# Optimization experiments

Hardware: AMD Instinct MI355X
Metric: run time of the kernel (lower is better)

The kernel has to match this reference:

```python
import jax, jax.numpy as jnp
import numpy as np

B, S, H, NH = 4, 2048, 512, 8
HD = H // NH  # head dim = 64


def setup_inputs() -> dict:
    key = jax.random.key(0)
    ks = jax.random.split(key, 12)
    f = lambda k, sh: jax.random.normal(k, sh, dtype=jnp.float32)
    w = lambda k: f(k, (H, H)) * 0.02  # Linear weight (out, in), torch-style
    return {
        "q": f(ks[0], (B, S, H)),
        "k": f(ks[1], (B, S, H)),
        "v": f(ks[2], (B, S, H)),
        "mask": jax.random.randint(ks[3], (B, S, S), 0, 2, dtype=jnp.int32),
        "Wq": w(ks[4]), "bq": jnp.zeros((H,), jnp.float32),
        "Wk": w(ks[5]), "bk": jnp.zeros((H,), jnp.float32),
        "Wv": w(ks[6]), "bv": jnp.zeros((H,), jnp.float32),
        "Wo": w(ks[7]), "bo": jnp.zeros((H,), jnp.float32),
    }


def reference(q, k, v, mask, Wq, bq, Wk, bk, Wv, bv, Wo, bo):
    b, s, h = q.shape
    scale = jnp.asarray(np.sqrt(HD), q.dtype)
    # QKV projections (torch Linear: x @ W.T + b), split into heads: b n s h
    def heads(x, W, bias):
        y = x @ W.T + bias
        return y.reshape(b, s, NH, HD).transpose(0, 2, 1, 3)
    Q = heads(q, Wq, bq)
    K = heads(k, Wk, bk)
    V = heads(v, Wv, bv)
    scores = jnp.einsum('bnsh,bnth->bnst', Q, K) / scale
    scores = jnp.where(mask[:, None, :, :] == 0, jnp.asarray(-1e9, scores.dtype), scores)
    attn = jax.nn.softmax(scores, axis=-1)
    # dropout is identity in eval mode
    out = jnp.einsum('bnst,bnth->bnsh', attn, V)
    out = out.transpose(0, 2, 1, 3).reshape(b, s, h)
    return out @ Wo.T + bo
```

## Files before the change

kernel.cpp:

```cpp
#include <hip/hip_runtime.h>
#include <cstdint>


typedef __bf16 bf16x8 __attribute__((ext_vector_type(8)));
typedef float  f32x4  __attribute__((ext_vector_type(4)));
typedef float  f32x16 __attribute__((ext_vector_type(16)));
typedef unsigned int uint32x2 __attribute__((ext_vector_type(2)));

#define MFMA16(a, b, c) __builtin_amdgcn_mfma_f32_16x16x32_bf16(a, b, c, 0, 0, 0)
#define MFMA32(a, b, c) __builtin_amdgcn_mfma_f32_32x32x16_bf16(a, b, c, 0, 0, 0)

__device__ __forceinline__ ushort f2bf(float f) {
  union { float f; uint32_t u; } v; v.f = f;
  return (ushort)((v.u + 0x8000u) >> 16);
}
__device__ __forceinline__ uint packbf(float a, float b) {
  union { float f; uint32_t u; } x, y; x.f = a; y.f = b;
#if __has_builtin(__builtin_amdgcn_perm)
  return __builtin_amdgcn_perm(y.u + 0x8000u, x.u + 0x8000u, 0x07060302u);
#else
  return ((x.u + 0x8000u) >> 16) | ((y.u + 0x8000u) & 0xffff0000u);
#endif
}
__device__ __forceinline__ uint cvtpk(float a, float b) {
  uint r;
  asm("v_cvt_pk_bf16_f32 %0, %1, %2" : "=v"(r) : "v"(a), "v"(b));
  return r;
}
__device__ __forceinline__ float exp2r(float x) {
#if __has_builtin(__builtin_amdgcn_exp2f)
  return __builtin_amdgcn_exp2f(x);
#else
  return exp2f(x);
#endif
}

typedef const __attribute__((address_space(1))) unsigned int* gas_u32;
typedef __attribute__((address_space(3))) unsigned int* las_u32;
__device__ __forceinline__ void gll16(const void* g, void* l) {
  __builtin_amdgcn_global_load_lds((gas_u32)g, (las_u32)l, 16, 0, 0);
}

__global__ __launch_bounds__(256) void cvt_w(
    const float* __restrict__ w0, const float* __restrict__ w1,
    const float* __restrict__ w2, const float* __restrict__ w3,
    ushort* __restrict__ dst) {
  const float* src = (blockIdx.y == 0) ? w0 : (blockIdx.y == 1) ? w1
                   : (blockIdx.y == 2) ? w2 : w3;
  ushort* d = dst + (size_t)blockIdx.y * 262144;
  int i = blockIdx.x * 256 + threadIdx.x;
  for (int j = i; j < 65536; j += 16384) {
    float4 v = ((const float4*)src)[j];
    uint2 o = { packbf(v.x, v.y), packbf(v.z, v.w) };
    ((uint2*)d)[j] = o;
  }
}

__global__ __launch_bounds__(256) void cvt_x(
    const float* __restrict__ q, const float* __restrict__ k,
    const float* __restrict__ v, ushort* __restrict__ dst) {
  const float* src = (blockIdx.y == 0) ? q : (blockIdx.y == 1) ? k : v;
  ushort* d = dst + (size_t)blockIdx.y * 4194304;
  int i = blockIdx.x * 256 + threadIdx.x;
  for (int j = i; j < 1048576; j += 65536) {
    float4 vv = ((const float4*)src)[j];
    uint2 o = { cvtpk(vv.x, vv.y), cvtpk(vv.z, vv.w) };
    ((uint2*)d)[j] = o;
  }
}

__global__ __launch_bounds__(256) void mask_bits_kernel(
    const int* __restrict__ mask, unsigned long long* __restrict__ MB) {
  const int lane = threadIdx.x & 63;
  const int wv = (int)((blockIdx.x * 256 + threadIdx.x) >> 6);
  const size_t base = (size_t)wv * 64;
  for (int j = 0; j < 64; j += 4) {
    int v0 = mask[(base + j + 0) * 64 + lane];
    int v1 = mask[(base + j + 1) * 64 + lane];
    int v2 = mask[(base + j + 2) * 64 + lane];
    int v3 = mask[(base + j + 3) * 64 + lane];
    unsigned long long b0 = __ballot(v0 != 0), b1 = __ballot(v1 != 0);
    unsigned long long b2 = __ballot(v2 != 0), b3 = __ballot(v3 != 0);
    if (lane == 0) {
      MB[base + j] = b0; MB[base + j + 1] = b1;
      MB[base + j + 2] = b2; MB[base + j + 3] = b3;
    }
  }
}

__global__ __launch_bounds__(256, 4) void qkv_gemm(
    const ushort* __restrict__ Xb, const ushort* __restrict__ Wb,
    const float* __restrict__ bq, const float* __restrict__ bk,
    const float* __restrict__ bv, ushort* __restrict__ Qh,
    ushort* __restrict__ Kh, ushort* __restrict__ Vt) {
  __shared__ ushort SM[16384];
  ushort* As = SM;
  ushort* Wt = SM + 8192;
  const int z = blockIdx.z;
  const ushort* X = Xb + (size_t)z * 4194304;
  const ushort* W = Wb + (size_t)z * 262144;
  const float* bias = (z == 0) ? bq : (z == 1) ? bk : bv;
  const float scale = (z == 0) ? 0.18033688011112042f : 1.0f;
  ushort* Y = (z == 0) ? Qh : (z == 1) ? Kh : Vt;

  const int tid = threadIdx.x, wv = tid >> 6, l = tid & 63;
  const int quad = l >> 4, ln = l & 15;
  const int m0 = blockIdx.x * 128, n0 = blockIdx.y * 128;
  const int wm = (wv & 1) * 64, wn = (wv >> 1) * 64;
  const int sr = l >> 3, sc = l & 7;
  f32x4 acc[4][4] = {};

  for (int kk = 0; kk < 512; kk += 64) {
#pragma unroll
    for (int i = 0; i < 4; ++i) {
      int row = wv * 32 + i * 8 + sr;
      gll16(X + (size_t)(m0 + row) * 512 + kk + ((sc ^ (row & 7)) * 8),
            As + (wv * 32 + i * 8) * 64);
      gll16(W + (size_t)(n0 + row) * 512 + kk + ((sc ^ (row & 7)) * 8),
            Wt + (wv * 32 + i * 8) * 64);
    }
    __syncthreads();
#pragma unroll
    for (int ks = 0; ks < 2; ++ks) {
      bf16x8 a[4], bw[4];
#pragma unroll
      for (int mt = 0; mt < 4; ++mt) {
        int row = wm + mt * 16 + ln;
        a[mt] = *(const bf16x8*)&As[row * 64 + (((ks * 4 + quad) ^ (row & 7)) * 8)];
      }
#pragma unroll
      for (int nt = 0; nt < 4; ++nt) {
        int row = wn + nt * 16 + ln;
        bw[nt] = *(const bf16x8*)&Wt[row * 64 + (((ks * 4 + quad) ^ (row & 7)) * 8)];
      }
#pragma unroll
      for (int mt = 0; mt < 4; ++mt)
#pragma unroll
        for (int nt = 0; nt < 4; ++nt)
          acc[mt][nt] = MFMA16(a[mt], bw[nt], acc[mt][nt]);
    }
    __syncthreads();
  }
  float bval[4];
#pragma unroll
  for (int nt = 0; nt < 4; ++nt) bval[nt] = bias[n0 + wn + nt * 16 + ln];

  if (z == 2) {
    ushort* uT = SM;
#pragma unroll
    for (int nt = 0; nt < 4; ++nt) {
      int row = wn + nt * 16 + ln;
#pragma unroll
      for (int mt = 0; mt < 4; ++mt) {
        int mbase = wm + mt * 16 + quad * 4;
        uint2 pk = { cvtpk(acc[mt][nt][0] + bval[nt], acc[mt][nt][1] + bval[nt]),
                     cvtpk(acc[mt][nt][2] + bval[nt], acc[mt][nt][3] + bval[nt]) };
        int c = (mbase >> 3) ^ (row & 7);
        *(uint2*)&uT[row * 128 + c * 8 + (quad & 1) * 4] = pk;
      }
    }
    __syncthreads();
#pragma unroll
    for (int j = 0; j < 8; ++j) {
      int i = tid + j * 256;
      int row = i >> 4, cs = i & 15;
      int g = cs ^ (row & 7);
      uint4 d = *(const uint4*)&uT[row * 128 + cs * 8];
      int n = n0 + row, m = m0 + g * 8;
      int bb = m >> 11, s = m & 2047, h = n >> 6, hd = n & 63;
      *(uint4*)(Y + ((size_t)((bb * 8 + h) * 64 + hd)) * 2048 + s) = d;
    }
  } else {
    ushort* uM = SM;
#pragma unroll
    for (int half = 0; half < 2; ++half) {
      __syncthreads();
      if ((wv >> 1) == half) {
#pragma unroll
        for (int mt = 0; mt < 4; ++mt)
#pragma unroll
          for (int nt = 0; nt < 4; ++nt) {
            int n = nt * 16 + ln;
#pragma unroll
            for (int r = 0; r < 4; ++r) {
              int m = wm + mt * 16 + quad * 4 + r;
              uM[m * 68 + n] = f2bf((acc[mt][nt][r] + bval[nt]) * scale);
            }
          }
      }
      __syncthreads();
#pragma unroll
      for (int j = 0; j < 4; ++j) {
        int i = tid + j * 256;
        int row = i >> 3, cs = i & 7;
        uint4 d = *(const uint4*)&uM[row * 68 + cs * 8];
        int m = m0 + row, n = n0 + half * 64 + cs * 8;
        int bb = m >> 11, s = m & 2047, h = n >> 6, hd = n & 63;
        *(uint4*)(Y + (((size_t)(bb * 8 + h) * 2048) + s) * 64 + hd) = d;
      }
    }
  }
}

__global__ __launch_bounds__(256, 4) void attn(
    const ushort* __restrict__ Qh, const ushort* __restrict__ Kh,
    const ushort* __restrict__ Vt, const unsigned long long* __restrict__ MB,
    ushort* __restrict__ O) {
  __shared__ ushort SMEM[16384];
  ushort* Ks = SMEM;
  ushort* Vs = SMEM + 8192;
  const int tid = threadIdx.x, wv = tid >> 6, lane = tid & 63;
  const int hs = lane >> 5, lq = lane & 31;
  const int qh = wv >> 1, kvh = wv & 1;
  const int bh = blockIdx.x, qb = blockIdx.y;
  const size_t hoff = (size_t)bh * 2048 * 64;
  const int q0 = qb * 64;
  const int qg = q0 + qh * 32 + lq;
  const int srK = lane >> 3, scK = lane & 7;
  const int srV = lane >> 4, scV = lane & 15;

  bf16x8 qf[4];
#pragma unroll
  for (int ki = 0; ki < 4; ++ki)
    qf[ki] = *(const bf16x8*)(Qh + hoff + (size_t)qg * 64 + ki * 16 + hs * 8);

  bf16x8 ones;
#pragma unroll
  for (int j = 0; j < 8; ++j) ones[j] = (__bf16)1.0f;

  f32x16 po0 = {}, po1 = {};
  f32x16 lacc = {};
  const unsigned long long* mrow = MB + ((size_t)(bh >> 3) * 2048 + qg) * 32;

  for (int it = 0; it < 16; ++it) {
    const int kv0 = it * 128;
#pragma unroll
    for (int i = 0; i < 4; ++i) {
      int row = wv * 32 + i * 8 + srK;
      gll16(Kh + hoff + (size_t)(kv0 + row) * 64 + ((scK ^ (row & 7)) * 8),
            Ks + (wv * 32 + i * 8) * 64);
      int rv = wv * 16 + i * 4 + srV;
      gll16(Vt + hoff + (size_t)rv * 2048 + kv0 + ((scV ^ (rv & 7)) * 8),
            Vs + (wv * 16 + i * 4) * 128);
    }
    unsigned long long mbw = mrow[it * 2 + kvh];
    __syncthreads();

#pragma unroll
    for (int ch = 0; ch < 2; ++ch) {
      const int kvb = kvh * 64 + ch * 32;
      f32x16 sc_ = {};
#pragma unroll
      for (int ki = 0; ki < 4; ++ki) {
        int row = kvb + lq;
        bf16x8 ak = *(const bf16x8*)&Ks[row * 64 + (((2 * ki + hs) ^ (row & 7)) * 8)];
        sc_ = MFMA32(ak, qf[ki], sc_);
      }
      uint pk[8];
#pragma unroll
      for (int c = 0; c < 4; ++c) {
        unsigned nib = (unsigned)(mbw >> (ch * 32 + c * 8 + hs * 4)) & 0xFu;
        float p0 = (nib & 1u) ? exp2r(sc_[4 * c + 0]) : 0.f;
        float p1 = (nib & 2u) ? exp2r(sc_[4 * c + 1]) : 0.f;
        float p2 = (nib & 4u) ? exp2r(sc_[4 * c + 2]) : 0.f;
        float p3 = (nib & 8u) ? exp2r(sc_[4 * c + 3]) : 0.f;
        pk[2 * c + 0] = cvtpk(p0, p1);
        pk[2 * c + 1] = cvtpk(p2, p3);
      }
#pragma unroll
      for (int t2 = 0; t2 < 2; ++t2) {
        union { uint u[4]; bf16x8 v; } bp;
#if __has_builtin(__builtin_amdgcn_permlane32_swap)
        uint32x2 r02 = __builtin_amdgcn_permlane32_swap(pk[4 * t2 + 0], pk[4 * t2 + 2], false, false);
        uint32x2 r13 = __builtin_amdgcn_permlane32_swap(pk[4 * t2 + 1], pk[4 * t2 + 3], false, false);
        bp.u[0] = r02[0];
        bp.u[1] = r13[0];
        bp.u[2] = r02[1];
        bp.u[3] = r13[1];
#else
        uint bx0 = (uint)__shfl_xor((int)(hs ? pk[4 * t2 + 0] : pk[4 * t2 + 2]), 32);
        uint bx1 = (uint)__shfl_xor((int)(hs ? pk[4 * t2 + 1] : pk[4 * t2 + 3]), 32);
        bp.u[0] = hs ? bx0 : pk[4 * t2 + 0];
        bp.u[1] = hs ? bx1 : pk[4 * t2 + 1];
        bp.u[2] = hs ? pk[4 * t2 + 2] : bx0;
        bp.u[3] = hs ? pk[4 * t2 + 3] : bx1;
#endif
        lacc = MFMA32(ones, bp.v, lacc);
#pragma unroll
        for (int m2 = 0; m2 < 2; ++m2) {
          int hd = m2 * 32 + lq;
          int gch = (kvb >> 3) + 2 * t2 + hs;
          bf16x8 av = *(const bf16x8*)&Vs[hd * 128 + ((gch ^ (hd & 7)) * 8)];
          if (m2 == 0) po0 = MFMA32(av, bp.v, po0);
          else         po1 = MFMA32(av, bp.v, po1);
        }
      }
    }
    __syncthreads();
  }

  float l_own = lacc[0];
  float* psh = (float*)Ks;
  float* lsh = (float*)Vs;
  ushort* Osh = Vs + 256;
  if (kvh == 1) {
#pragma unroll
    for (int i = 0; i < 16; ++i) psh[(qh * 32 + i) * 64 + lane] = po0[i];
#pragma unroll
    for (int i = 0; i < 16; ++i) psh[(qh * 32 + 16 + i) * 64 + lane] = po1[i];
    lsh[qh * 64 + lane] = l_own;
  }
  __syncthreads();
  if (kvh == 0) {
    float linv = 1.0f / (l_own + lsh[qh * 64 + lane]);
    int row = qh * 32 + lq;
#pragma unroll
    for (int m2 = 0; m2 < 2; ++m2) {
#pragma unroll
      for (int c = 0; c < 4; ++c)
#pragma unroll
        for (int b2 = 0; b2 < 2; ++b2) {
          int r = 4 * c + 2 * b2;
          float v0, v1;
          if (m2 == 0) {
            v0 = (po0[r] + psh[(qh * 32 + r) * 64 + lane]) * linv;
            v1 = (po0[r + 1] + psh[(qh * 32 + r + 1) * 64 + lane]) * linv;
          } else {
            v0 = (po1[r] + psh[(qh * 32 + 16 + r) * 64 + lane]) * linv;
            v1 = (po1[r + 1] + psh[(qh * 32 + 16 + r + 1) * 64 + lane]) * linv;
          }
          int hd = m2 * 32 + 8 * c + 4 * hs + 2 * b2;
          *(uint*)&Osh[row * 72 + hd] = cvtpk(v0, v1);
        }
    }
  }
  __syncthreads();
  for (int i = tid; i < 512; i += 256) {
    int row = i >> 3, cc = i & 7;
    uint4 d = *(const uint4*)&Osh[row * 72 + cc * 8];
    *(uint4*)(O + ((size_t)((bh >> 3) * 2048 + q0 + row)) * 512 +
              (bh & 7) * 64 + cc * 8) = d;
  }
}

__global__ __launch_bounds__(256) void out_gemm(
    const ushort* __restrict__ X, const ushort* __restrict__ W,
    const float* __restrict__ bias, float* __restrict__ Y) {
  __shared__ ushort As[64 * 64];
  __shared__ ushort Ws[128 * 64];
  const int tid = threadIdx.x, wv = tid >> 6, l = tid & 63;
  const int quad = l >> 4, ln = l & 15;
  const int m0 = blockIdx.x * 64, n0 = blockIdx.y * 128;
  const int wm = (wv & 1) * 32, wn = (wv >> 1) * 64;
  const int sr = l >> 3, sc = l & 7;
  f32x4 acc[2][4] = {};
  for (int kk = 0; kk < 512; kk += 64) {
#pragma unroll
    for (int i = 0; i < 2; ++i) {
      int row = wv * 16 + i * 8 + sr;
      gll16(X + (size_t)(m0 + row) * 512 + kk + ((sc ^ (row & 7)) * 8),
            As + (wv * 16 + i * 8) * 64);
    }
#pragma unroll
    for (int i = 0; i < 4; ++i) {
      int row = wv * 32 + i * 8 + sr;
      gll16(W + (size_t)(n0 + row) * 512 + kk + ((sc ^ (row & 7)) * 8),
            Ws + (wv * 32 + i * 8) * 64);
    }
    __syncthreads();
#pragma unroll
    for (int ks = 0; ks < 2; ++ks) {
      bf16x8 a[2], bw[4];
#pragma unroll
      for (int mt = 0; mt < 2; ++mt) {
        int row = wm + mt * 16 + ln;
        a[mt] = *(const bf16x8*)&As[row * 64 + (((ks * 4 + quad) ^ (row & 7)) * 8)];
      }
#pragma unroll
      for (int nt = 0; nt < 4; ++nt) {
        int row = wn + nt * 16 + ln;
        bw[nt] = *(const bf16x8*)&Ws[row * 64 + (((ks * 4 + quad) ^ (row & 7)) * 8)];
      }
#pragma unroll
      for (int mt = 0; mt < 2; ++mt)
#pragma unroll
        for (int nt = 0; nt < 4; ++nt)
          acc[mt][nt] = MFMA16(a[mt], bw[nt], acc[mt][nt]);
    }
    __syncthreads();
  }
#pragma unroll
  for (int mt = 0; mt < 2; ++mt)
#pragma unroll
    for (int nt = 0; nt < 4; ++nt) {
      int n = n0 + wn + nt * 16 + ln;
      float bval = bias[n];
#pragma unroll
      for (int r = 0; r < 4; ++r) {
        int m = m0 + wm + mt * 16 + quad * 4 + r;
        Y[(size_t)m * 512 + n] = acc[mt][nt][r] + bval;
      }
    }
}

extern "C" void kernel_launch(void* const* d_in, const int* in_sizes, int n_in,
                              void* d_out, int out_size, void* d_ws, size_t ws_size,
                              hipStream_t stream) {
  const float* q    = (const float*)d_in[0];
  const float* k    = (const float*)d_in[1];
  const float* v    = (const float*)d_in[2];
  const int*   mask = (const int*)d_in[3];
  const float* Wq   = (const float*)d_in[4];
  const float* bq   = (const float*)d_in[5];
  const float* Wk   = (const float*)d_in[6];
  const float* bk   = (const float*)d_in[7];
  const float* Wv   = (const float*)d_in[8];
  const float* bv   = (const float*)d_in[9];
  const float* Wo   = (const float*)d_in[10];
  const float* bo   = (const float*)d_in[11];
  float* out = (float*)d_out;

  uint8_t* ws = (uint8_t*)d_ws;
  const size_t MiB = 1u << 20;
  ushort* Oh = (ushort*)(ws + 0 * MiB);
  ushort* Qh = (ushort*)(ws + 8 * MiB);
  ushort* Kh = (ushort*)(ws + 16 * MiB);
  ushort* Vt = (ushort*)(ws + 24 * MiB);
  unsigned long long* MB = (unsigned long long*)(ws + 32 * MiB);
  ushort* Wb = (ushort*)(ws + 34 * MiB);
  ushort* Xb = (ushort*)(ws + 36 * MiB);

  cvt_w<<<dim3(64, 4), 256, 0, stream>>>(Wq, Wk, Wv, Wo, Wb);
  cvt_x<<<dim3(256, 3), 256, 0, stream>>>(q, k, v, Xb);
  mask_bits_kernel<<<1024, 256, 0, stream>>>(mask, MB);
  qkv_gemm<<<dim3(64, 4, 3), 256, 0, stream>>>(Xb, Wb, bq, bk, bv, Qh, Kh, Vt);
  attn<<<dim3(32, 32), 256, 0, stream>>>(Qh, Kh, Vt, MB, Oh);
  out_gemm<<<dim3(128, 4), 256, 0, stream>>>(Oh, Wb + 3 * 262144, bo, out);
}
```

Before: 261.5 us.

## Fuse all stages into one persistent kernel with grid-wide atomic barriers

Merges the conversion, mask packing, QKV GEMM, attention and output GEMM kernels into a single 1024-block launch whose phases are separated by a software grid barrier built on an atomic counter and spinning. This removes per-launch overhead and the gaps between the six kernels. It relies on all 1024 blocks being co-resident (256 CUs at four blocks per CU); otherwise the barrier deadlocks. Barrier spin cost and the lost overlap between independent stages are the trade-offs.

```diff
diff --git a/kernel.cpp b/kernel.cpp
--- a/kernel.cpp
+++ b/kernel.cpp
@@ -13,14 +13,6 @@
 __device__ __forceinline__ ushort f2bf(float f) {
   union { float f; uint32_t u; } v; v.f = f;
   return (ushort)((v.u + 0x8000u) >> 16);
-}
-__device__ __forceinline__ uint packbf(float a, float b) {
-  union { float f; uint32_t u; } x, y; x.f = a; y.f = b;
-#if __has_builtin(__builtin_amdgcn_perm)
-  return __builtin_amdgcn_perm(y.u + 0x8000u, x.u + 0x8000u, 0x07060302u);
-#else
-  return ((x.u + 0x8000u) >> 16) | ((y.u + 0x8000u) & 0xffff0000u);
-#endif
 }
 __device__ __forceinline__ uint cvtpk(float a, float b) {
   uint r;
@@ -41,366 +33,378 @@
   __builtin_amdgcn_global_load_lds((gas_u32)g, (las_u32)l, 16, 0, 0);
 }
 
-__global__ __launch_bounds__(256) void cvt_w(
-    const float* __restrict__ w0, const float* __restrict__ w1,
-    const float* __restrict__ w2, const float* __restrict__ w3,
-    ushort* __restrict__ dst) {
-  const float* src = (blockIdx.y == 0) ? w0 : (blockIdx.y == 1) ? w1
-                   : (blockIdx.y == 2) ? w2 : w3;
-  ushort* d = dst + (size_t)blockIdx.y * 262144;
-  int i = blockIdx.x * 256 + threadIdx.x;
-  for (int j = i; j < 65536; j += 16384) {
-    float4 v = ((const float4*)src)[j];
-    uint2 o = { packbf(v.x, v.y), packbf(v.z, v.w) };
-    ((uint2*)d)[j] = o;
+__device__ __forceinline__ void gbar(unsigned* bar, int tid) {
+  __syncthreads();
+  if (tid == 0) {
+    __threadfence();
+    unsigned old = atomicAdd(bar, 1u);
+    unsigned target = (old / 1024u + 1u) * 1024u;
+    while (__hip_atomic_load(bar, __ATOMIC_RELAXED, __HIP_MEMORY_SCOPE_AGENT) < target)
+      __builtin_amdgcn_s_sleep(2);
   }
-}
-
-__global__ __launch_bounds__(256) void cvt_x(
+  __syncthreads();
+  __threadfence();
+}
+
+__global__ __launch_bounds__(256, 4) void mega(
     const float* __restrict__ q, const float* __restrict__ k,
-    const float* __restrict__ v, ushort* __restrict__ dst) {
-  const float* src = (blockIdx.y == 0) ? q : (blockIdx.y == 1) ? k : v;
-  ushort* d = dst + (size_t)blockIdx.y * 4194304;
-  int i = blockIdx.x * 256 + threadIdx.x;
-  for (int j = i; j < 1048576; j += 65536) {
-    float4 vv = ((const float4*)src)[j];
-    uint2 o = { cvtpk(vv.x, vv.y), cvtpk(vv.z, vv.w) };
-    ((uint2*)d)[j] = o;
+    const float* __restrict__ v, const int* __restrict__ mask,
+    const float* __restrict__ Wq, const float* __restrict__ bq,
+    const float* __restrict__ Wk, const float* __restrict__ bk,
+    const float* __restrict__ Wv, const float* __restrict__ bv,
+    const float* __restrict__ Wo, const float* __restrict__ bo,
+    float* __restrict__ out, ushort* __restrict__ Oh,
+    ushort* __restrict__ Qh, ushort* __restrict__ Kh,
+    ushort* __restrict__ Vt, unsigned long long* __restrict__ MB,
+    ushort* __restrict__ Wb, ushort* __restrict__ Xb,
+    unsigned* __restrict__ bar) {
+  __shared__ ushort SM[16384];
+  const int bid = blockIdx.x, tid = threadIdx.x;
+  const int wv = tid >> 6, l = tid & 63;
+
+  {
+    int i = bid * 256 + tid;
+    {
+      int wsel = i >> 16, j = i & 65535;
+      const float* src = (wsel == 0) ? Wq : (wsel == 1) ? Wk
+                       : (wsel == 2) ? Wv : Wo;
+      float4 vv = ((const float4*)src)[j];
+      uint2 o = { cvtpk(vv.x, vv.y), cvtpk(vv.z, vv.w) };
+      ((uint2*)(Wb + (size_t)wsel * 262144))[j] = o;
+    }
+#pragma unroll
+    for (int t = 0; t < 12; ++t) {
+      int g = i + t * 262144;
+      int zsel = g >> 20, j = g & 1048575;
+      const float* src = (zsel == 0) ? q : (zsel == 1) ? k : v;
+      float4 vv = ((const float4*)src)[j];
+      uint2 o = { cvtpk(vv.x, vv.y), cvtpk(vv.z, vv.w) };
+      ((uint2*)(Xb + (size_t)zsel * 4194304))[j] = o;
+    }
+    const int lane = l;
+    const int wvg = i >> 6;
+    const size_t base = (size_t)wvg * 64;
+    for (int j = 0; j < 64; j += 4) {
+      int v0 = mask[(base + j + 0) * 64 + lane];
+      int v1 = mask[(base + j + 1) * 64 + lane];
+      int v2 = mask[(base + j + 2) * 64 + lane];
+      int v3 = mask[(base + j + 3) * 64 + lane];
+      unsigned long long b0 = __ballot(v0 != 0), b1 = __ballot(v1 != 0);
+      unsigned long long b2 = __ballot(v2 != 0), b3 = __ballot(v3 != 0);
+      if (lane == 0) {
+        MB[base + j] = b0; MB[base + j + 1] = b1;
+        MB[base + j + 2] = b2; MB[base + j + 3] = b3;
+      }
+    }
   }
-}
-
-__global__ __launch_bounds__(256) void mask_bits_kernel(
-    const int* __restrict__ mask, unsigned long long* __restrict__ MB) {
-  const int lane = threadIdx.x & 63;
-  const int wv = (int)((blockIdx.x * 256 + threadIdx.x) >> 6);
-  const size_t base = (size_t)wv * 64;
-  for (int j = 0; j < 64; j += 4) {
-    int v0 = mask[(base + j + 0) * 64 + lane];
-    int v1 = mask[(base + j + 1) * 64 + lane];
-    int v2 = mask[(base + j + 2) * 64 + lane];
-    int v3 = mask[(base + j + 3) * 64 + lane];
-    unsigned long long b0 = __ballot(v0 != 0), b1 = __ballot(v1 != 0);
-    unsigned long long b2 = __ballot(v2 != 0), b3 = __ballot(v3 != 0);
-    if (lane == 0) {
-      MB[base + j] = b0; MB[base + j + 1] = b1;
-      MB[base + j + 2] = b2; MB[base + j + 3] = b3;
-    }
-  }
-}
-
-__global__ __launch_bounds__(256, 4) void qkv_gemm(
-    const ushort* __restrict__ Xb, const ushort* __restrict__ Wb,
-    const float* __restrict__ bq, const float* __restrict__ bk,
-    const float* __restrict__ bv, ushort* __restrict__ Qh,
-    ushort* __restrict__ Kh, ushort* __restrict__ Vt) {
-  __shared__ ushort SM[16384];
-  ushort* As = SM;
-  ushort* Wt = SM + 8192;
-  const int z = blockIdx.z;
-  const ushort* X = Xb + (size_t)z * 4194304;
-  const ushort* W = Wb + (size_t)z * 262144;
-  const float* bias = (z == 0) ? bq : (z == 1) ? bk : bv;
-  const float scale = (z == 0) ? 0.18033688011112042f : 1.0f;
-  ushort* Y = (z == 0) ? Qh : (z == 1) ? Kh : Vt;
-
-  const int tid = threadIdx.x, wv = tid >> 6, l = tid & 63;
-  const int quad = l >> 4, ln = l & 15;
-  const int m0 = blockIdx.x * 128, n0 = blockIdx.y * 128;
-  const int wm = (wv & 1) * 64, wn = (wv >> 1) * 64;
-  const int sr = l >> 3, sc = l & 7;
-  f32x4 acc[4][4] = {};
-
-  for (int kk = 0; kk < 512; kk += 64) {
-#pragma unroll
-    for (int i = 0; i < 4; ++i) {
-      int row = wv * 32 + i * 8 + sr;
-      gll16(X + (size_t)(m0 + row) * 512 + kk + ((sc ^ (row & 7)) * 8),
-            As + (wv * 32 + i * 8) * 64);
-      gll16(W + (size_t)(n0 + row) * 512 + kk + ((sc ^ (row & 7)) * 8),
-            Wt + (wv * 32 + i * 8) * 64);
-    }
-    __syncthreads();
-#pragma unroll
-    for (int ks = 0; ks < 2; ++ks) {
-      bf16x8 a[4], bw[4];
-#pragma unroll
-      for (int mt = 0; mt < 4; ++mt) {
-        int row = wm + mt * 16 + ln;
-        a[mt] = *(const bf16x8*)&As[row * 64 + (((ks * 4 + quad) ^ (row & 7)) * 8)];
-      }
+  gbar(bar, tid);
+
+  if (bid < 768) {
+    ushort* As = SM;
+    ushort* Wt = SM + 8192;
+    const int z = bid >> 8, rr = bid & 255;
+    const int bx = rr & 63, by = rr >> 6;
+    const ushort* X = Xb + (size_t)z * 4194304;
+    const ushort* W = Wb + (size_t)z * 262144;
+    const float* bias = (z == 0) ? bq : (z == 1) ? bk : bv;
+    const float scale = (z == 0) ? 0.18033688011112042f : 1.0f;
+    ushort* Y = (z == 0) ? Qh : (z == 1) ? Kh : Vt;
+
+    const int quad = l >> 4, ln = l & 15;
+    const int m0 = bx * 128, n0 = by * 128;
+    const int wm = (wv & 1) * 64, wn = (wv >> 1) * 64;
+    const int sr = l >> 3, sc = l & 7;
+    f32x4 acc[4][4] = {};
+
+    for (int kk = 0; kk < 512; kk += 64) {
+#pragma unroll
+      for (int i = 0; i < 4; ++i) {
+        int row = wv * 32 + i * 8 + sr;
+        gll16(X + (size_t)(m0 + row) * 512 + kk + ((sc ^ (row & 7)) * 8),
+              As + (wv * 32 + i * 8) * 64);
+        gll16(W + (size_t)(n0 + row) * 512 + kk + ((sc ^ (row & 7)) * 8),
+              Wt + (wv * 32 + i * 8) * 64);
+      }
+      __syncthreads();
+#pragma unroll
+      for (int ks = 0; ks < 2; ++ks) {
+        bf16x8 a[4], bw[4];
+#pragma unroll
+        for (int mt = 0; mt < 4; ++mt) {
+          int row = wm + mt * 16 + ln;
+          a[mt] = *(const bf16x8*)&As[row * 64 + (((ks * 4 + quad) ^ (row & 7)) * 8)];
+        }
+#pragma unroll
+        for (int nt = 0; nt < 4; ++nt) {
+          int row = wn + nt * 16 + ln;
+          bw[nt] = *(const bf16x8*)&Wt[row * 64 + (((ks * 4 + quad) ^ (row & 7)) * 8)];
+        }
+#pragma unroll
+        for (int mt = 0; mt < 4; ++mt)
+#pragma unroll
+          for (int nt = 0; nt < 4; ++nt)
+            acc[mt][nt] = MFMA16(a[mt], bw[nt], acc[mt][nt]);
+      }
+      __syncthreads();
+    }
+    float bval[4];
+#pragma unroll
+    for (int nt = 0; nt < 4; ++nt) bval[nt] = bias[n0 + wn + nt * 16 + ln];
+
+    if (z == 2) {
+      ushort* uT = SM;
 #pragma unroll
       for (int nt = 0; nt < 4; ++nt) {
         int row = wn + nt * 16 + ln;
-        bw[nt] = *(const bf16x8*)&Wt[row * 64 + (((ks * 4 + quad) ^ (row & 7)) * 8)];
-      }
-#pragma unroll
-      for (int mt = 0; mt < 4; ++mt)
-#pragma unroll
-        for (int nt = 0; nt < 4; ++nt)
-          acc[mt][nt] = MFMA16(a[mt], bw[nt], acc[mt][nt]);
+#pragma unroll
+        for (int mt = 0; mt < 4; ++mt) {
+          int mbase = wm + mt * 16 + quad * 4;
+          uint2 pk = { cvtpk(acc[mt][nt][0] + bval[nt], acc[mt][nt][1] + bval[nt]),
+                       cvtpk(acc[mt][nt][2] + bval[nt], acc[mt][nt][3] + bval[nt]) };
+          int c = (mbase >> 3) ^ (row & 7);
+          *(uint2*)&uT[row * 128 + c * 8 + (quad & 1) * 4] = pk;
+        }
+      }
+      __syncthreads();
+#pragma unroll
+      for (int j = 0; j < 8; ++j) {
+        int i = tid + j * 256;
+        int row = i >> 4, cs = i & 15;
+        int g = cs ^ (row & 7);
+        uint4 d = *(const uint4*)&uT[row * 128 + cs * 8];
+        int n = n0 + row, m = m0 + g * 8;
+        int bb = m >> 11, s = m & 2047, h = n >> 6, hd = n & 63;
+        *(uint4*)(Y + ((size_t)((bb * 8 + h) * 64 + hd)) * 2048 + s) = d;
+      }
+    } else {
+      ushort* uM = SM;
+#pragma unroll
+      for (int half = 0; half < 2; ++half) {
+        __syncthreads();
+        if ((wv >> 1) == half) {
+#pragma unroll
+          for (int mt = 0; mt < 4; ++mt)
+#pragma unroll
+            for (int nt = 0; nt < 4; ++nt) {
+              int n = nt * 16 + ln;
+#pragma unroll
+              for (int r = 0; r < 4; ++r) {
+                int m = wm + mt * 16 + quad * 4 + r;
+                uM[m * 68 + n] = f2bf((acc[mt][nt][r] + bval[nt]) * scale);
+              }
+            }
+        }
+        __syncthreads();
+#pragma unroll
+        for (int j = 0; j < 4; ++j) {
+          int i = tid + j * 256;
+          int row = i >> 3, cs = i & 7;
+          uint4 d = *(const uint4*)&uM[row * 68 + cs * 8];
+          int m = m0 + row, n = n0 + half * 64 + cs * 8;
+          int bb = m >> 11, s = m & 2047, h = n >> 6, hd = n & 63;
+          *(uint4*)(Y + (((size_t)(bb * 8 + h) * 2048) + s) * 64 + hd) = d;
+        }
+      }
+    }
+  }
+  gbar(bar, tid);
+
+  {
+    ushort* Ks = SM;
+    ushort* Vs = SM + 8192;
+    const int lane = l;
+    const int hs = lane >> 5, lq = lane & 31;
+    const int qh = wv >> 1, kvh = wv & 1;
+    const int bh = bid & 31, qb = bid >> 5;
+    const size_t hoff = (size_t)bh * 2048 * 64;
+    const int q0 = qb * 64;
+    const int qg = q0 + qh * 32 + lq;
+    const int srK = lane >> 3, scK = lane & 7;
+    const int srV = lane >> 4, scV = lane & 15;
+
+    bf16x8 qf[4];
+#pragma unroll
+    for (int ki = 0; ki < 4; ++ki)
+      qf[ki] = *(const bf16x8*)(Qh + hoff + (size_t)qg * 64 + ki * 16 + hs * 8);
+
+    bf16x8 ones;
+#pragma unroll
+    for (int j = 0; j < 8; ++j) ones[j] = (__bf16)1.0f;
+
+    f32x16 po0 = {}, po1 = {};
+    f32x16 lacc = {};
+    const unsigned long long* mrow = MB + ((size_t)(bh >> 3) * 2048 + qg) * 32;
+
+    for (int it = 0; it < 16; ++it) {
+      const int kv0 = it * 128;
+#pragma unroll
+      for (int i = 0; i < 4; ++i) {
+        int row = wv * 32 + i * 8 + srK;
+        gll16(Kh + hoff + (size_t)(kv0 + row) * 64 + ((scK ^ (row & 7)) * 8),
+              Ks + (wv * 32 + i * 8) * 64);
+        int rv = wv * 16 + i * 4 + srV;
+        gll16(Vt + hoff + (size_t)rv * 2048 + kv0 + ((scV ^ (rv & 7)) * 8),
+              Vs + (wv * 16 + i * 4) * 128);
+      }
+      unsigned long long mbw = mrow[it * 2 + kvh];
+      __syncthreads();
+
+#pragma unroll
+      for (int ch = 0; ch < 2; ++ch) {
+        const int kvb = kvh * 64 + ch * 32;
+        f32x16 sc_ = {};
+#pragma unroll
+        for (int ki = 0; ki < 4; ++ki) {
+          int row = kvb + lq;
+          bf16x8 ak = *(const bf16x8*)&Ks[row * 64 + (((2 * ki + hs) ^ (row & 7)) * 8)];
+          sc_ = MFMA32(ak, qf[ki], sc_);
+        }
+        uint pk[8];
+#pragma unroll
+        for (int c = 0; c < 4; ++c) {
+          unsigned nib = (unsigned)(mbw >> (ch * 32 + c * 8 + hs * 4)) & 0xFu;
+          float p0 = (nib & 1u) ? exp2r(sc_[4 * c + 0]) : 0.f;
+          float p1 = (nib & 2u) ? exp2r(sc_[4 * c + 1]) : 0.f;
+          float p2 = (nib & 4u) ? exp2r(sc_[4 * c + 2]) : 0.f;
+          float p3 = (nib & 8u) ? exp2r(sc_[4 * c + 3]) : 0.f;
+          pk[2 * c + 0] = cvtpk(p0, p1);
+          pk[2 * c + 1] = cvtpk(p2, p3);
+        }
+#pragma unroll
+        for (int t2 = 0; t2 < 2; ++t2) {
+          union { uint u[4]; bf16x8 v; } bp;
+#if __has_builtin(__builtin_amdgcn_permlane32_swap)
+          uint32x2 r02 = __builtin_amdgcn_permlane32_swap(pk[4 * t2 + 0], pk[4 * t2 + 2], false, false);
+          uint32x2 r13 = __builtin_amdgcn_permlane32_swap(pk[4 * t2 + 1], pk[4 * t2 + 3], false, false);
+          bp.u[0] = r02[0];
+          bp.u[1] = r13[0];
+          bp.u[2] = r02[1];
+          bp.u[3] = r13[1];
+#else
+          uint bx0 = (uint)__shfl_xor((int)(hs ? pk[4 * t2 + 0] : pk[4 * t2 + 2]), 32);
+          uint bx1 = (uint)__shfl_xor((int)(hs ? pk[4 * t2 + 1] : pk[4 * t2 + 3]), 32);
+          bp.u[0] = hs ? bx0 : pk[4 * t2 + 0];
+          bp.u[1] = hs ? bx1 : pk[4 * t2 + 1];
+          bp.u[2] = hs ? pk[4 * t2 + 2] : bx0;
+          bp.u[3] = hs ? pk[4 * t2 + 3] : bx1;
+#endif
+          lacc = MFMA32(ones, bp.v, lacc);
+#pragma unroll
+          for (int m2 = 0; m2 < 2; ++m2) {
+            int hd = m2 * 32 + lq;
+            int gch = (kvb >> 3) + 2 * t2 + hs;
+            bf16x8 av = *(const bf16x8*)&Vs[hd * 128 + ((gch ^ (hd & 7)) * 8)];
+            if (m2 == 0) po0 = MFMA32(av, bp.v, po0);
+            else         po1 = MFMA32(av, bp.v, po1);
+          }
+        }
+      }
+      __syncthreads();
+    }
+
+    float l_own = lacc[0];
+    float* psh = (float*)Ks;
+    float* lsh = (float*)Vs;
+    ushort* Osh = Vs + 256;
+    if (kvh == 1) {
+#pragma unroll
+      for (int i = 0; i < 16; ++i) psh[(qh * 32 + i) * 64 + lane] = po0[i];
+#pragma unroll
+      for (int i = 0; i < 16; ++i) psh[(qh * 32 + 16 + i) * 64 + lane] = po1[i];
+      lsh[qh * 64 + lane] = l_own;
     }
     __syncthreads();
+    if (kvh == 0) {
+      float linv = 1.0f / (l_own + lsh[qh * 64 + lane]);
+      int row = qh * 32 + lq;
+#pragma unroll
+      for (int m2 = 0; m2 < 2; ++m2) {
+#pragma unroll
+        for (int c = 0; c < 4; ++c)
+#pragma unroll
+          for (int b2 = 0; b2 < 2; ++b2) {
+            int r = 4 * c + 2 * b2;
+            float v0, v1;
+            if (m2 == 0) {
+              v0 = (po0[r] + psh[(qh * 32 + r) * 64 + lane]) * linv;
+              v1 = (po0[r + 1] + psh[(qh * 32 + r + 1) * 64 + lane]) * linv;
+            } else {
+              v0 = (po1[r] + psh[(qh * 32 + 16 + r) * 64 + lane]) * linv;
+              v1 = (po1[r + 1] + psh[(qh * 32 + 16 + r + 1) * 64 + lane]) * linv;
+            }
+            int hd = m2 * 32 + 8 * c + 4 * hs + 2 * b2;
+            *(uint*)&Osh[row * 72 + hd] = cvtpk(v0, v1);
+          }
+      }
+    }
+    __syncthreads();
+    for (int i = tid; i < 512; i += 256) {
+      int row = i >> 3, cc = i & 7;
+      uint4 d = *(const uint4*)&Osh[row * 72 + cc * 8];
+      *(uint4*)(Oh + ((size_t)((bh >> 3) * 2048 + q0 + row)) * 512 +
+                (bh & 7) * 64 + cc * 8) = d;
+    }
   }
-  float bval[4];
-#pragma unroll
-  for (int nt = 0; nt < 4; ++nt) bval[nt] = bias[n0 + wn + nt * 16 + ln];
-
-  if (z == 2) {
-    ushort* uT = SM;
-#pragma unroll
-    for (int nt = 0; nt < 4; ++nt) {
-      int row = wn + nt * 16 + ln;
-#pragma unroll
-      for (int mt = 0; mt < 4; ++mt) {
-        int mbase = wm + mt * 16 + quad * 4;
-        uint2 pk = { cvtpk(acc[mt][nt][0] + bval[nt], acc[mt][nt][1] + bval[nt]),
-                     cvtpk(acc[mt][nt][2] + bval[nt], acc[mt][nt][3] + bval[nt]) };
-        int c = (mbase >> 3) ^ (row & 7);
-        *(uint2*)&uT[row * 128 + c * 8 + (quad & 1) * 4] = pk;
-      }
-    }
-    __syncthreads();
-#pragma unroll
-    for (int j = 0; j < 8; ++j) {
-      int i = tid + j * 256;
-      int row = i >> 4, cs = i & 15;
-      int g = cs ^ (row & 7);
-      uint4 d = *(const uint4*)&uT[row * 128 + cs * 8];
-      int n = n0 + row, m = m0 + g * 8;
-      int bb = m >> 11, s = m & 2047, h = n >> 6, hd = n & 63;
-      *(uint4*)(Y + ((size_t)((bb * 8 + h) * 64 + hd)) * 2048 + s) = d;
-    }
-  } else {
-    ushort* uM = SM;
-#pragma unroll
-    for (int half = 0; half < 2; ++half) {
-      __syncthreads();
-      if ((wv >> 1) == half) {
-#pragma unroll
-        for (int mt = 0; mt < 4; ++mt)
-#pragma unroll
-          for (int nt = 0; nt < 4; ++nt) {
-            int n = nt * 16 + ln;
-#pragma unroll
-            for (int r = 0; r < 4; ++r) {
-              int m = wm + mt * 16 + quad * 4 + r;
-              uM[m * 68 + n] = f2bf((acc[mt][nt][r] + bval[nt]) * scale);
-            }
-          }
-      }
-      __syncthreads();
-#pragma unroll
-      for (int j = 0; j < 4; ++j) {
-        int i = tid + j * 256;
-        int row = i >> 3, cs = i & 7;
-        uint4 d = *(const uint4*)&uM[row * 68 + cs * 8];
-        int m = m0 + row, n = n0 + half * 64 + cs * 8;
-        int bb = m >> 11, s = m & 2047, h = n >> 6, hd = n & 63;
-        *(uint4*)(Y + (((size_t)(bb * 8 + h) * 2048) + s) * 64 + hd) = d;
-      }
-    }
+  gbar(bar, tid);
+
+  if (bid < 512) {
+    ushort* As = SM;
+    ushort* Ws = SM + 4096;
+    const ushort* W = Wb + 3 * 262144;
+    const int bx = bid & 127, by = bid >> 7;
+    const int quad = l >> 4, ln = l & 15;
+    const int m0 = bx * 64, n0 = by * 128;
+    const int wm = (wv & 1) * 32, wn = (wv >> 1) * 64;
+    const int sr = l >> 3, sc = l & 7;
+    f32x4 acc[2][4] = {};
+    for (int kk = 0; kk < 512; kk += 64) {
+#pragma unroll
+      for (int i = 0; i < 2; ++i) {
+        int row = wv * 16 + i * 8 + sr;
+        gll16(Oh + (size_t)(m0 + row) * 512 + kk + ((sc ^ (row & 7)) * 8),
+              As + (wv * 16 + i * 8) * 64);
+      }
+#pragma unroll
+      for (int i = 0; i < 4; ++i) {
+        int row = wv * 32 + i * 8 + sr;
+        gll16(W + (size_t)(n0 + row) * 512 + kk + ((sc ^ (row & 7)) * 8),
+              Ws + (wv * 32 + i * 8) * 64);
+      }
+      __syncthreads();
+#pragma unroll
+      for (int ks = 0; ks < 2; ++ks) {
+        bf16x8 a[2], bw[4];
+#pragma unroll
+        for (int mt = 0; mt < 2; ++mt) {
+          int row = wm + mt * 16 + ln;
+          a[mt] = *(const bf16x8*)&As[row * 64 + (((ks * 4 + quad) ^ (row & 7)) * 8)];
+        }
+#pragma unroll
+        for (int nt = 0; nt < 4; ++nt) {
+          int row = wn + nt * 16 + ln;
+          bw[nt] = *(const bf16x8*)&Ws[row * 64 + (((ks * 4 + quad) ^ (row & 7)) * 8)];
+        }
+#pragma unroll
+        for (int mt = 0; mt < 2; ++mt)
+#pragma unroll
+          for (int nt = 0; nt < 4; ++nt)
+            acc[mt][nt] = MFMA16(a[mt], bw[nt], acc[mt][nt]);
+      }
+      __syncthreads();
+    }
+#pragma unroll
+    for (int mt = 0; mt < 2; ++mt)
+#pragma unroll
+      for (int nt = 0; nt < 4; ++nt) {
+        int n = n0 + wn + nt * 16 + ln;
+        float bval = bo[n];
+#pragma unroll
+        for (int r = 0; r < 4; ++r) {
+          int m = m0 + wm + mt * 16 + quad * 4 + r;
+          out[(size_t)m * 512 + n] = acc[mt][nt][r] + bval;
+        }
+      }
   }
-}
-
-__global__ __launch_bounds__(256, 4) void attn(
-    const ushort* __restrict__ Qh, const ushort* __restrict__ Kh,
-    const ushort* __restrict__ Vt, const unsigned long long* __restrict__ MB,
-    ushort* __restrict__ O) {
-  __shared__ ushort SMEM[16384];
-  ushort* Ks = SMEM;
-  ushort* Vs = SMEM + 8192;
-  const int tid = threadIdx.x, wv = tid >> 6, lane = tid & 63;
-  const int hs = lane >> 5, lq = lane & 31;
-  const int qh = wv >> 1, kvh = wv & 1;
-  const int bh = blockIdx.x, qb = blockIdx.y;
-  const size_t hoff = (size_t)bh * 2048 * 64;
-  const int q0 = qb * 64;
-  const int qg = q0 + qh * 32 + lq;
-  const int srK = lane >> 3, scK = lane & 7;
-  const int srV = lane >> 4, scV = lane & 15;
-
-  bf16x8 qf[4];
-#pragma unroll
-  for (int ki = 0; ki < 4; ++ki)
-    qf[ki] = *(const bf16x8*)(Qh + hoff + (size_t)qg * 64 + ki * 16 + hs * 8);
-
-  bf16x8 ones;
-#pragma unroll
-  for (int j = 0; j < 8; ++j) ones[j] = (__bf16)1.0f;
-
-  f32x16 po0 = {}, po1 = {};
-  f32x16 lacc = {};
-  const unsigned long long* mrow = MB + ((size_t)(bh >> 3) * 2048 + qg) * 32;
-
-  for (int it = 0; it < 16; ++it) {
-    const int kv0 = it * 128;
-#pragma unroll
-    for (int i = 0; i < 4; ++i) {
-      int row = wv * 32 + i * 8 + srK;
-      gll16(Kh + hoff + (size_t)(kv0 + row) * 64 + ((scK ^ (row & 7)) * 8),
-            Ks + (wv * 32 + i * 8) * 64);
-      int rv = wv * 16 + i * 4 + srV;
-      gll16(Vt + hoff + (size_t)rv * 2048 + kv0 + ((scV ^ (rv & 7)) * 8),
-            Vs + (wv * 16 + i * 4) * 128);
-    }
-    unsigned long long mbw = mrow[it * 2 + kvh];
-    __syncthreads();
-
-#pragma unroll
-    for (int ch = 0; ch < 2; ++ch) {
-      const int kvb = kvh * 64 + ch * 32;
-      f32x16 sc_ = {};
-#pragma unroll
-      for (int ki = 0; ki < 4; ++ki) {
-        int row = kvb + lq;
-        bf16x8 ak = *(const bf16x8*)&Ks[row * 64 + (((2 * ki + hs) ^ (row & 7)) * 8)];
-        sc_ = MFMA32(ak, qf[ki], sc_);
-      }
-      uint pk[8];
-#pragma unroll
-      for (int c = 0; c < 4; ++c) {
-        unsigned nib = (unsigned)(mbw >> (ch * 32 + c * 8 + hs * 4)) & 0xFu;
-        float p0 = (nib & 1u) ? exp2r(sc_[4 * c + 0]) : 0.f;
-        float p1 = (nib & 2u) ? exp2r(sc_[4 * c + 1]) : 0.f;
-        float p2 = (nib & 4u) ? exp2r(sc_[4 * c + 2]) : 0.f;
-        float p3 = (nib & 8u) ? exp2r(sc_[4 * c + 3]) : 0.f;
-        pk[2 * c + 0] = cvtpk(p0, p1);
-        pk[2 * c + 1] = cvtpk(p2, p3);
-      }
-#pragma unroll
-      for (int t2 = 0; t2 < 2; ++t2) {
-        union { uint u[4]; bf16x8 v; } bp;
-#if __has_builtin(__builtin_amdgcn_permlane32_swap)
-        uint32x2 r02 = __builtin_amdgcn_permlane32_swap(pk[4 * t2 + 0], pk[4 * t2 + 2], false, false);
-        uint32x2 r13 = __builtin_amdgcn_permlane32_swap(pk[4 * t2 + 1], pk[4 * t2 + 3], false, false);
-        bp.u[0] = r02[0];
-        bp.u[1] = r13[0];
-        bp.u[2] = r02[1];
-        bp.u[3] = r13[1];
-#else
-        uint bx0 = (uint)__shfl_xor((int)(hs ? pk[4 * t2 + 0] : pk[4 * t2 + 2]), 32);
-        uint bx1 = (uint)__shfl_xor((int)(hs ? pk[4 * t2 + 1] : pk[4 * t2 + 3]), 32);
-        bp.u[0] = hs ? bx0 : pk[4 * t2 + 0];
-        bp.u[1] = hs ? bx1 : pk[4 * t2 + 1];
-        bp.u[2] = hs ? pk[4 * t2 + 2] : bx0;
-        bp.u[3] = hs ? pk[4 * t2 + 3] : bx1;
-#endif
-        lacc = MFMA32(ones, bp.v, lacc);
-#pragma unroll
-        for (int m2 = 0; m2 < 2; ++m2) {
-          int hd = m2 * 32 + lq;
-          int gch = (kvb >> 3) + 2 * t2 + hs;
-          bf16x8 av = *(const bf16x8*)&Vs[hd * 128 + ((gch ^ (hd & 7)) * 8)];
-          if (m2 == 0) po0 = MFMA32(av, bp.v, po0);
-          else         po1 = MFMA32(av, bp.v, po1);
-        }
-      }
-    }
-    __syncthreads();
-  }
-
-  float l_own = lacc[0];
-  float* psh = (float*)Ks;
-  float* lsh = (float*)Vs;
-  ushort* Osh = Vs + 256;
-  if (kvh == 1) {
-#pragma unroll
-    for (int i = 0; i < 16; ++i) psh[(qh * 32 + i) * 64 + lane] = po0[i];
-#pragma unroll
-    for (int i = 0; i < 16; ++i) psh[(qh * 32 + 16 + i) * 64 + lane] = po1[i];
-    lsh[qh * 64 + lane] = l_own;
-  }
-  __syncthreads();
-  if (kvh == 0) {
-    float linv = 1.0f / (l_own + lsh[qh * 64 + lane]);
-    int row = qh * 32 + lq;
-#pragma unroll
-    for (int m2 = 0; m2 < 2; ++m2) {
-#pragma unroll
-      for (int c = 0; c < 4; ++c)
-#pragma unroll
-        for (int b2 = 0; b2 < 2; ++b2) {
-          int r = 4 * c + 2 * b2;
-          float v0, v1;
-          if (m2 == 0) {
-            v0 = (po0[r] + psh[(qh * 32 + r) * 64 + lane]) * linv;
-            v1 = (po0[r + 1] + psh[(qh * 32 + r + 1) * 64 + lane]) * linv;
-          } else {
-            v0 = (po1[r] + psh[(qh * 32 + 16 + r) * 64 + lane]) * linv;
-            v1 = (po1[r + 1] + psh[(qh * 32 + 16 + r + 1) * 64 + lane]) * linv;
-          }
-          int hd = m2 * 32 + 8 * c + 4 * hs + 2 * b2;
-          *(uint*)&Osh[row * 72 + hd] = cvtpk(v0, v1);
-        }
-    }
-  }
-  __syncthreads();
-  for (int i = tid; i < 512; i += 256) {
-    int row = i >> 3, cc = i & 7;
-    uint4 d = *(const uint4*)&Osh[row * 72 + cc * 8];
-    *(uint4*)(O + ((size_t)((bh >> 3) * 2048 + q0 + row)) * 512 +
-              (bh & 7) * 64 + cc * 8) = d;
-  }
-}
-
-__global__ __launch_bounds__(256) void out_gemm(
-    const ushort* __restrict__ X, const ushort* __restrict__ W,
-    const float* __restrict__ bias, float* __restrict__ Y) {
-  __shared__ ushort As[64 * 64];
-  __shared__ ushort Ws[128 * 64];
-  const int tid = threadIdx.x, wv = tid >> 6, l = tid & 63;
-  const int quad = l >> 4, ln = l & 15;
-  const int m0 = blockIdx.x * 64, n0 = blockIdx.y * 128;
-  const int wm = (wv & 1) * 32, wn = (wv >> 1) * 64;
-  const int sr = l >> 3, sc = l & 7;
-  f32x4 acc[2][4] = {};
-  for (int kk = 0; kk < 512; kk += 64) {
-#pragma unroll
-    for (int i = 0; i < 2; ++i) {
-      int row = wv * 16 + i * 8 + sr;
-      gll16(X + (size_t)(m0 + row) * 512 + kk + ((sc ^ (row & 7)) * 8),
-            As + (wv * 16 + i * 8) * 64);
-    }
-#pragma unroll
-    for (int i = 0; i < 4; ++i) {
-      int row = wv * 32 + i * 8 + sr;
-      gll16(W + (size_t)(n0 + row) * 512 + kk + ((sc ^ (row & 7)) * 8),
-            Ws + (wv * 32 + i * 8) * 64);
-    }
-    __syncthreads();
-#pragma unroll
-    for (int ks = 0; ks < 2; ++ks) {
-      bf16x8 a[2], bw[4];
-#pragma unroll
-      for (int mt = 0; mt < 2; ++mt) {
-        int row = wm + mt * 16 + ln;
-        a[mt] = *(const bf16x8*)&As[row * 64 + (((ks * 4 + quad) ^ (row & 7)) * 8)];
-      }
-#pragma unroll
-      for (int nt = 0; nt < 4; ++nt) {
-        int row = wn + nt * 16 + ln;
-        bw[nt] = *(const bf16x8*)&Ws[row * 64 + (((ks * 4 + quad) ^ (row & 7)) * 8)];
-      }
-#pragma unroll
-      for (int mt = 0; mt < 2; ++mt)
-#pragma unroll
-        for (int nt = 0; nt < 4; ++nt)
-          acc[mt][nt] = MFMA16(a[mt], bw[nt], acc[mt][nt]);
-    }
-    __syncthreads();
-  }
-#pragma unroll
-  for (int mt = 0; mt < 2; ++mt)
-#pragma unroll
-    for (int nt = 0; nt < 4; ++nt) {
-      int n = n0 + wn + nt * 16 + ln;
-      float bval = bias[n];
-#pragma unroll
-      for (int r = 0; r < 4; ++r) {
-        int m = m0 + wm + mt * 16 + quad * 4 + r;
-        Y[(size_t)m * 512 + n] = acc[mt][nt][r] + bval;
-      }
-    }
 }
 
 extern "C" void kernel_launch(void* const* d_in, const int* in_sizes, int n_in,
@@ -429,11 +433,10 @@
   unsigned long long* MB = (unsigned long long*)(ws + 32 * MiB);
   ushort* Wb = (ushort*)(ws + 34 * MiB);
   ushort* Xb = (ushort*)(ws + 36 * MiB);
-
-  cvt_w<<<dim3(64, 4), 256, 0, stream>>>(Wq, Wk, Wv, Wo, Wb);
-  cvt_x<<<dim3(256, 3), 256, 0, stream>>>(q, k, v, Xb);
-  mask_bits_kernel<<<1024, 256, 0, stream>>>(mask, MB);
-  qkv_gemm<<<dim3(64, 4, 3), 256, 0, stream>>>(Xb, Wb, bq, bk, bv, Qh, Kh, Vt);
-  attn<<<dim3(32, 32), 256, 0, stream>>>(Qh, Kh, Vt, MB, Oh);
-  out_gemm<<<dim3(128, 4), 256, 0, stream>>>(Oh, Wb + 3 * 262144, bo, out);
-}
+  unsigned* bar = (unsigned*)(ws + 60 * MiB);
+
+  hipMemsetAsync(bar, 0, 16, stream);
+  mega<<<dim3(1024), dim3(256), 0, stream>>>(
+      q, k, v, mask, Wq, bq, Wk, bk, Wv, bv, Wo, bo,
+      out, Oh, Qh, Kh, Vt, MB, Wb, Xb, bar);
+}
```

Result: slower. 759.4 us (+190.5%).
